# Kernel tuning notes

Measured on AMD Instinct MI355X. Metric: run time of the kernel, lower is better.

Reference implementation:

```python
import jax, jax.numpy as jnp
import numpy as np

M = 8192      # nodes
D = 128       # feature dim
DEG = 32      # neighbors per node


def setup_inputs() -> dict:
    key = jax.random.key(0)
    ks = jax.random.split(key, 6)
    z = jax.random.normal(ks[0], (M, D), dtype=jnp.float32)
    # deterministic, duplicate-free edge list: node i -> (i+1..i+DEG) mod M
    src = jnp.repeat(jnp.arange(M, dtype=jnp.int64), DEG)
    dst = (src + jnp.tile(jnp.arange(1, DEG + 1, dtype=jnp.int64), M)) % M
    edge_index = jnp.stack([src, dst], axis=0)  # [2, M*DEG]
    s = 1.0 / np.sqrt(D)
    Wg = jax.random.normal(ks[1], (D, D), dtype=jnp.float32) * s
    Wc = jax.random.normal(ks[2], (D, D), dtype=jnp.float32) * s
    Wq = jax.random.normal(ks[3], (D, D), dtype=jnp.float32) * s
    Wk = jax.random.normal(ks[4], (D, D), dtype=jnp.float32) * s
    a = jax.random.normal(ks[5], (2 * D,), dtype=jnp.float32)
    return {"z": z, "edge_index": edge_index, "Wg": Wg, "Wc": Wc,
            "Wq": Wq, "Wk": Wk, "a": a}


def reference(z, edge_index, Wg, Wc, Wq, Wk, a):
    m, d = z.shape
    wg = z @ Wg.T                              # [m, d]
    src, dst = edge_index[0], edge_index[1]
    a_src, a_dst = a[:d], a[d:]
    # per-edge score: leaky_relu(a . [wg[i], wg[j]]) = leaky_relu(a1.wg[i] + a2.wg[j])
    scores = jax.nn.leaky_relu((wg @ a_src)[src] + (wg @ a_dst)[dst])  # [E]
    # softmax over each source node's neighbors (segment softmax)
    smax = jax.ops.segment_max(scores, src, num_segments=m)
    ex = jnp.exp(scores - smax[src])
    denom = jax.ops.segment_sum(ex, src, num_segments=m)
    alpha = ex / denom[src]                    # [E]
    # scatter-aggregate: local[i] = sum_j alpha_ij * wg[j]
    local = jax.ops.segment_sum(alpha[:, None] * wg[dst], src, num_segments=m)
    # dense global attention branch
    q = z @ Wq.T
    k = z @ Wk.T
    beta = jax.nn.softmax(q @ k.T / jnp.sqrt(jnp.float32(d)), axis=-1)  # [m, m]
    global_msg = beta @ (z @ Wc.T)
    return jax.nn.leaky_relu(local + global_msg + z)
```

## Files before the change

### kernel.cpp

```cpp
#include <hip/hip_runtime.h>

#define MM 8192
#define DD 128
#define DEG 32
#define KSPLIT 8
#define BK 64
#define NTILE 16
#define NB 16
#define RSTAGE 48

typedef __attribute__((ext_vector_type(8))) _Float16 h8;
typedef __attribute__((ext_vector_type(4))) float f4;
typedef __attribute__((ext_vector_type(4))) unsigned int u4;
typedef __attribute__((ext_vector_type(4))) short s4;

__device__ __forceinline__ unsigned short f2h(float f) {
  _Float16 h = (_Float16)f;
  return __builtin_bit_cast(unsigned short, h);
}

__device__ __forceinline__ void lds_dma16(const unsigned short* gptr, unsigned short* lptr) {
  __builtin_amdgcn_global_load_lds(
      (const __attribute__((address_space(1))) unsigned int*)gptr,
      (__attribute__((address_space(3))) unsigned int*)lptr, 16, 0, 0);
}

__global__ __launch_bounds__(256) void proj_kernel(
    const float* __restrict__ z, const float* __restrict__ Wg,
    const float* __restrict__ Wc, const float* __restrict__ Wq,
    const float* __restrict__ Wk, const float* __restrict__ a,
    float* __restrict__ wg, unsigned short* __restrict__ qb,
    unsigned short* __restrict__ kb, unsigned short* __restrict__ ct,
    float* __restrict__ sg, float* __restrict__ sd)
{
  __shared__ unsigned short zt[64 * 136];
  __shared__ unsigned short wt[128 * 136];
  const int mode = blockIdx.y;
  const float* __restrict__ W = (mode == 0) ? Wg : (mode == 1) ? Wq : (mode == 2) ? Wk : Wc;
  const int r0 = blockIdx.x * 64;
  const int tid = threadIdx.x;

  #pragma unroll
  for (int it = 0; it < 8; ++it) {
    int id = tid + it * 256, row = id >> 5, c4 = (id & 31) * 4;
    f4 v = *(const f4*)(z + (r0 + row) * DD + c4);
    s4 sv = {(short)f2h(v.x), (short)f2h(v.y), (short)f2h(v.z), (short)f2h(v.w)};
    *(s4*)&zt[row * 136 + c4] = sv;
  }
  #pragma unroll
  for (int it = 0; it < 16; ++it) {
    int id = tid + it * 256, row = id >> 5, c4 = (id & 31) * 4;
    f4 v = *(const f4*)(W + row * DD + c4);
    s4 sv = {(short)f2h(v.x), (short)f2h(v.y), (short)f2h(v.z), (short)f2h(v.w)};
    *(s4*)&wt[row * 136 + c4] = sv;
  }
  __syncthreads();

  const int lane = tid & 63, w = tid >> 6, n = lane & 15, quad = lane >> 4;
  h8 afr[4];
  #pragma unroll
  for (int kt = 0; kt < 4; ++kt)
    afr[kt] = *(const h8*)&zt[(16 * w + n) * 136 + kt * 32 + quad * 8];

  f4 acc[8];
  const f4 fzero = {0.f, 0.f, 0.f, 0.f};
  #pragma unroll
  for (int nt = 0; nt < 8; ++nt) {
    f4 c = fzero;
    #pragma unroll
    for (int kt = 0; kt < 4; ++kt) {
      h8 b = *(const h8*)&wt[(16 * nt + n) * 136 + kt * 32 + quad * 8];
      c = __builtin_amdgcn_mfma_f32_16x16x32_f16(afr[kt], b, c, 0, 0, 0);
    }
    acc[nt] = c;
  }

  if (mode == 0) {
    #pragma unroll
    for (int nt = 0; nt < 8; ++nt)
      #pragma unroll
      for (int r = 0; r < 4; ++r)
        wg[(r0 + 16 * w + quad * 4 + r) * DD + 16 * nt + n] = acc[nt][r];
    float av[8], bv[8];
    #pragma unroll
    for (int nt = 0; nt < 8; ++nt) { av[nt] = a[16 * nt + n]; bv[nt] = a[DD + 16 * nt + n]; }
    #pragma unroll
    for (int r = 0; r < 4; ++r) {
      float s1 = 0.f, s2 = 0.f;
      #pragma unroll
      for (int nt = 0; nt < 8; ++nt) { s1 += acc[nt][r] * av[nt]; s2 += acc[nt][r] * bv[nt]; }
      s1 += __shfl_xor(s1, 1); s1 += __shfl_xor(s1, 2); s1 += __shfl_xor(s1, 4); s1 += __shfl_xor(s1, 8);
      s2 += __shfl_xor(s2, 1); s2 += __shfl_xor(s2, 2); s2 += __shfl_xor(s2, 4); s2 += __shfl_xor(s2, 8);
      if (n == 0) {
        int g = r0 + 16 * w + quad * 4 + r;
        sg[g] = s1; sd[g] = s2;
      }
    }
  } else if (mode == 1) {
    const float qscale = 0.12752551286084110f;
    #pragma unroll
    for (int nt = 0; nt < 8; ++nt)
      #pragma unroll
      for (int r = 0; r < 4; ++r)
        qb[(r0 + 16 * w + quad * 4 + r) * DD + 16 * nt + n] = f2h(acc[nt][r] * qscale);
  } else if (mode == 2) {
    #pragma unroll
    for (int nt = 0; nt < 8; ++nt)
      #pragma unroll
      for (int r = 0; r < 4; ++r)
        kb[(r0 + 16 * w + quad * 4 + r) * DD + 16 * nt + n] = f2h(acc[nt][r]);
  } else {
    __syncthreads();
    #pragma unroll
    for (int nt = 0; nt < 8; ++nt)
      #pragma unroll
      for (int r = 0; r < 4; ++r)
        wt[(16 * nt + n) * 80 + 16 * w + quad * 4 + r] = f2h(acc[nt][r]);
    __syncthreads();
    #pragma unroll
    for (int it = 0; it < 4; ++it) {
      int idx = tid + it * 256, d = idx >> 3, c8 = (idx & 7) * 8;
      u4 v = *(const u4*)&wt[d * 80 + c8];
      *(u4*)(ct + (size_t)d * MM + r0 + c8) = v;
    }
  }
}

__global__ __launch_bounds__(256, 2) void flash_kernel(
    const unsigned short* __restrict__ qb, const unsigned short* __restrict__ kb,
    const unsigned short* __restrict__ ct, unsigned short* __restrict__ Opart,
    float* __restrict__ Lpart)
{
  __shared__ unsigned short sh[37376];
  const int bid = blockIdx.x + (blockIdx.y << 6);
  const int ck = bid & 7, qt = bid >> 3;
  const int tid = threadIdx.x, lane = tid & 63, w = tid >> 6;
  const int n = lane & 15, quad = lane >> 4;
  const int qr0 = qt * 128;

  #pragma unroll
  for (int it = 0; it < 8; ++it)
    lds_dma16(qb + (qr0 + it * 16 + n) * DD + w * 32 + quad * 8,
              &sh[(it * 256 + tid) * 8]);
  __syncthreads();
  h8 aq[2][4];
  #pragma unroll
  for (int mt = 0; mt < 2; ++mt)
    #pragma unroll
    for (int kt = 0; kt < 4; ++kt)
      aq[mt][kt] = *(const h8*)&sh[((w * 2 + mt) * 4 + kt) * 512 + lane * 8];
  __syncthreads();

  const unsigned short* kp = kb + (size_t)(ck * 1024 + 4 * n) * DD + w * 32 + quad * 8;
  const unsigned short* vp = ct + (size_t)(16 * (w >> 1) + n) * MM + ck * 1024 + (w & 1) * 32 + quad * 8;

  #pragma unroll
  for (int it = 0; it < 4; ++it)
    lds_dma16(kp + it * DD, &sh[(it * 256 + tid) * 8]);
  #pragma unroll
  for (int it = 0; it < 4; ++it)
    lds_dma16(vp + (size_t)it * 32 * MM, &sh[8192 + (it * 256 + tid) * 8]);

  f4 acc_o[2][8];
  const f4 fzero = {0.f, 0.f, 0.f, 0.f};
  #pragma unroll
  for (int mt = 0; mt < 2; ++mt)
    #pragma unroll
    for (int dt = 0; dt < 8; ++dt) acc_o[mt][dt] = fzero;
  float l_r[2][4] = {{0.f, 0.f, 0.f, 0.f}, {0.f, 0.f, 0.f, 0.f}};
  const int pbase = 32768 + w * 1152;

  for (int t = 0; t < NTILE; ++t) {
    __syncthreads();
    const int cur = (t & 1) * 16384;

    if (t < NTILE - 1) {
      const int nb = ((t + 1) & 1) * 16384;
      const unsigned short* kpn = kp + (size_t)(t + 1) * BK * DD;
      const unsigned short* vpn = vp + (t + 1) * BK;
      #pragma unroll
      for (int it = 0; it < 4; ++it)
        lds_dma16(kpn + it * DD, &sh[nb + (it * 256 + tid) * 8]);
      #pragma unroll
      for (int it = 0; it < 4; ++it)
        lds_dma16(vpn + (size_t)it * 32 * MM, &sh[nb + 8192 + (it * 256 + tid) * 8]);
    }

    f4 accs[2][4];
    #pragma unroll
    for (int mt = 0; mt < 2; ++mt)
      #pragma unroll
      for (int nt = 0; nt < 4; ++nt) accs[mt][nt] = fzero;
    #pragma unroll
    for (int nt = 0; nt < 4; ++nt) {
      #pragma unroll
      for (int kt = 0; kt < 4; ++kt) {
        h8 bk = *(const h8*)&sh[cur + nt * 2048 + kt * 512 + lane * 8];
        accs[0][nt] = __builtin_amdgcn_mfma_f32_16x16x32_f16(aq[0][kt], bk, accs[0][nt], 0, 0, 0);
        accs[1][nt] = __builtin_amdgcn_mfma_f32_16x16x32_f16(aq[1][kt], bk, accs[1][nt], 0, 0, 0);
      }
    }

    h8 ap[2][2];
    #pragma unroll
    for (int mt = 0; mt < 2; ++mt) {
      #pragma unroll
      for (int r = 0; r < 4; ++r) {
        float p0 = exp2f(fminf(accs[mt][0][r], 14.4269504f));
        float p1 = exp2f(fminf(accs[mt][1][r], 14.4269504f));
        float p2 = exp2f(fminf(accs[mt][2][r], 14.4269504f));
        float p3 = exp2f(fminf(accs[mt][3][r], 14.4269504f));
        l_r[mt][r] += (p0 + p1) + (p2 + p3);
        auto pk0 = __builtin_amdgcn_cvt_pkrtz(p0, p1);
        auto pk1 = __builtin_amdgcn_cvt_pkrtz(p2, p3);
        uint2 pv2; pv2.x = __builtin_bit_cast(unsigned int, pk0);
        pv2.y = __builtin_bit_cast(unsigned int, pk1);
        *(uint2*)&sh[pbase + (quad * 4 + r) * 72 + n * 4] = pv2;
      }
      ap[mt][0] = *(const h8*)&sh[pbase + n * 72 + quad * 8];
      ap[mt][1] = *(const h8*)&sh[pbase + n * 72 + 32 + quad * 8];
    }

    #pragma unroll
    for (int dt = 0; dt < 8; ++dt) {
      #pragma unroll
      for (int k2 = 0; k2 < 2; ++k2) {
        h8 bv = *(const h8*)&sh[cur + 8192 + dt * 1024 + k2 * 512 + lane * 8];
        acc_o[0][dt] = __builtin_amdgcn_mfma_f32_16x16x32_f16(ap[0][k2], bv, acc_o[0][dt], 0, 0, 0);
        acc_o[1][dt] = __builtin_amdgcn_mfma_f32_16x16x32_f16(ap[1][k2], bv, acc_o[1][dt], 0, 0, 0);
      }
    }
  }

  #pragma unroll
  for (int mt = 0; mt < 2; ++mt)
    #pragma unroll
    for (int r = 0; r < 4; ++r) {
      float lv = l_r[mt][r];
      lv += __shfl_xor(lv, 1); lv += __shfl_xor(lv, 2);
      lv += __shfl_xor(lv, 4); lv += __shfl_xor(lv, 8);
      int g = qr0 + w * 32 + mt * 16 + quad * 4 + r;
      if (n == 0) __builtin_nontemporal_store(lv, &Lpart[ck * MM + g]);
      #pragma unroll
      for (int dt = 0; dt < 8; ++dt)
        __builtin_nontemporal_store(f2h(acc_o[mt][dt][r]),
                                    &Opart[((size_t)ck * MM + g) * DD + 16 * dt + n]);
    }
}

__global__ __launch_bounds__(256) void merge_kernel(
    const int* __restrict__ ei, const float* __restrict__ wg,
    const float* __restrict__ sg, const float* __restrict__ sd,
    const unsigned short* __restrict__ Opart, const float* __restrict__ Lpart,
    const float* __restrict__ z, float* __restrict__ out)
{
  __shared__ float rows_s[RSTAGE * 132];
  __shared__ float sc_s[NB][DEG];
  __shared__ float alpha_s[NB][DEG];
  __shared__ int idx_s[NB][DEG];
  const int tid = threadIdx.x;
  const int i0 = blockIdx.x * NB;

  #pragma unroll
  for (int it = 0; it < 6; ++it) {
    int idx = tid + it * 256;
    int r = idx >> 5, c4 = (idx & 31) * 4;
    int grow = (i0 + 1 + r) & (MM - 1);
    *(f4*)&rows_s[r * 132 + c4] = *(const f4*)(wg + (size_t)grow * DD + c4);
  }
  #pragma unroll
  for (int it = 0; it < 2; ++it) {
    int e = tid + it * 256;
    int nj = e >> 5, j = e & 31;
    int i = i0 + nj;
    int dstj = ei[MM * DEG + i * DEG + j];
    float s = sg[i] + sd[dstj];
    sc_s[nj][j] = s > 0.f ? s : 0.01f * s;
    idx_s[nj][j] = (dstj - (i0 + 1)) & (MM - 1);
  }
  __syncthreads();

  const int ni = tid >> 4, l16 = tid & 15;
  {
    float s0 = sc_s[ni][l16], s1 = sc_s[ni][l16 + 16];
    float mx = fmaxf(s0, s1);
    mx = fmaxf(mx, __shfl_xor(mx, 1)); mx = fmaxf(mx, __shfl_xor(mx, 2));
    mx = fmaxf(mx, __shfl_xor(mx, 4)); mx = fmaxf(mx, __shfl_xor(mx, 8));
    float p0 = __expf(s0 - mx), p1 = __expf(s1 - mx);
    float sum = p0 + p1;
    sum += __shfl_xor(sum, 1); sum += __shfl_xor(sum, 2);
    sum += __shfl_xor(sum, 4); sum += __shfl_xor(sum, 8);
    float inv = 1.f / sum;
    alpha_s[ni][l16] = p0 * inv;
    alpha_s[ni][l16 + 16] = p1 * inv;
  }

  const int d0 = l16 * 8;
  const int i = i0 + ni;
  float acc[8] = {0.f, 0.f, 0.f, 0.f, 0.f, 0.f, 0.f, 0.f};
  #pragma unroll 4
  for (int j = 0; j < DEG; ++j) {
    float al = alpha_s[ni][j];
    int r = idx_s[ni][j];
    if (r < RSTAGE) {
      const float* src = &rows_s[r * 132 + d0];
      #pragma unroll
      for (int q = 0; q < 8; ++q) acc[q] += al * src[q];
    } else {
      const float* src = wg + (size_t)((i0 + 1 + r) & (MM - 1)) * DD + d0;
      #pragma unroll
      for (int q = 0; q < 8; ++q) acc[q] += al * src[q];
    }
  }

  float l = 0.f;
  float o[8] = {0.f, 0.f, 0.f, 0.f, 0.f, 0.f, 0.f, 0.f};
  #pragma unroll
  for (int ck = 0; ck < KSPLIT; ++ck) {
    l += __builtin_nontemporal_load(&Lpart[ck * MM + i]);
    h8 v = __builtin_nontemporal_load((const h8*)(Opart + ((size_t)ck * MM + i) * DD + d0));
    #pragma unroll
    for (int q = 0; q < 8; ++q) o[q] += (float)v[q];
  }
  float inv = 1.0f / l;
  const float* zp = z + (size_t)i * DD + d0;
  float* op = out + (size_t)i * DD + d0;
  #pragma unroll
  for (int q = 0; q < 8; ++q) {
    float r = o[q] * inv + acc[q] + zp[q];
    op[q] = r > 0.f ? r : 0.01f * r;
  }
}

extern "C" void kernel_launch(void* const* d_in, const int* in_sizes, int n_in,
                              void* d_out, int out_size, void* d_ws, size_t ws_size,
                              hipStream_t stream) {
  const float* z  = (const float*)d_in[0];
  const int*   ei = (const int*)d_in[1];
  const float* Wg = (const float*)d_in[2];
  const float* Wc = (const float*)d_in[3];
  const float* Wq = (const float*)d_in[4];
  const float* Wk = (const float*)d_in[5];
  const float* a  = (const float*)d_in[6];
  float* out = (float*)d_out;
  char* ws = (char*)d_ws;

  float*          wg    = (float*)(ws + 0);
  unsigned short* qb    = (unsigned short*)(ws + (4 << 20));
  unsigned short* kb    = (unsigned short*)(ws + (6 << 20));
  unsigned short* ct    = (unsigned short*)(ws + (8 << 20));
  float*          sg    = (float*)(ws + (10 << 20));
  float*          sd    = (float*)(ws + (10 << 20) + (64 << 10));
  unsigned short* Opart = (unsigned short*)(ws + (11 << 20));
  float*          Lpart = (float*)(ws + (27 << 20));

  proj_kernel<<<dim3(128, 4), 256, 0, stream>>>(z, Wg, Wc, Wq, Wk, a, wg, qb, kb, ct, sg, sd);
  flash_kernel<<<dim3(64, KSPLIT), 256, 0, stream>>>(qb, kb, ct, Opart, Lpart);
  merge_kernel<<<512, 256, 0, stream>>>(ei, wg, sg, sd, Opart, Lpart, z, out);
}
```

Before: 133.4 us.

## Use packed fp16 conversion, regular stores, simpler flash grid, vectorized merge gather

Several small changes land together. The projection kernel now converts fp32 to fp16 with packed cvt_pkrtz (round toward zero) instead of per-element casts. The flash kernel takes its split index directly from blockIdx.y instead of decoding a flattened block id, which changes how blocks are ordered across the grid. Opart/Lpart stores and loads switch from nontemporal to regular accesses so the partials can stay in cache for the merge kernel, and the merge kernel's neighbor aggregation uses a single pointer select with f4 vector loads instead of a branch. The rounding mode of the z/W conversion changes slightly.

New measurement: 131.2 us. No clear change (-1.6%).

```diff
diff --git a/kernel.cpp b/kernel.cpp
--- a/kernel.cpp
+++ b/kernel.cpp
@@ -10,13 +10,17 @@
 #define RSTAGE 48
 
 typedef __attribute__((ext_vector_type(8))) _Float16 h8;
+typedef __attribute__((ext_vector_type(2))) _Float16 h2;
 typedef __attribute__((ext_vector_type(4))) float f4;
 typedef __attribute__((ext_vector_type(4))) unsigned int u4;
-typedef __attribute__((ext_vector_type(4))) short s4;
 
 __device__ __forceinline__ unsigned short f2h(float f) {
   _Float16 h = (_Float16)f;
   return __builtin_bit_cast(unsigned short, h);
+}
+
+__device__ __forceinline__ unsigned int pkrtz(float a, float b) {
+  return __builtin_bit_cast(unsigned int, __builtin_amdgcn_cvt_pkrtz(a, b));
 }
 
 __device__ __forceinline__ void lds_dma16(const unsigned short* gptr, unsigned short* lptr) {
@@ -44,15 +48,15 @@
   for (int it = 0; it < 8; ++it) {
     int id = tid + it * 256, row = id >> 5, c4 = (id & 31) * 4;
     f4 v = *(const f4*)(z + (r0 + row) * DD + c4);
-    s4 sv = {(short)f2h(v.x), (short)f2h(v.y), (short)f2h(v.z), (short)f2h(v.w)};
-    *(s4*)&zt[row * 136 + c4] = sv;
+    uint2 pk; pk.x = pkrtz(v.x, v.y); pk.y = pkrtz(v.z, v.w);
+    *(uint2*)&zt[row * 136 + c4] = pk;
   }
   #pragma unroll
   for (int it = 0; it < 16; ++it) {
     int id = tid + it * 256, row = id >> 5, c4 = (id & 31) * 4;
     f4 v = *(const f4*)(W + row * DD + c4);
-    s4 sv = {(short)f2h(v.x), (short)f2h(v.y), (short)f2h(v.z), (short)f2h(v.w)};
-    *(s4*)&wt[row * 136 + c4] = sv;
+    uint2 pk; pk.x = pkrtz(v.x, v.y); pk.y = pkrtz(v.z, v.w);
+    *(uint2*)&wt[row * 136 + c4] = pk;
   }
   __syncthreads();
 
@@ -132,15 +136,15 @@
     float* __restrict__ Lpart)
 {
   __shared__ unsigned short sh[37376];
-  const int bid = blockIdx.x + (blockIdx.y << 6);
-  const int ck = bid & 7, qt = bid >> 3;
+  const int bx = blockIdx.x, ck = blockIdx.y;
   const int tid = threadIdx.x, lane = tid & 63, w = tid >> 6;
   const int n = lane & 15, quad = lane >> 4;
-  const int qr0 = qt * 128;
+  const int ln = n, lq = quad;
+  const int qr0 = bx * 128;
 
   #pragma unroll
   for (int it = 0; it < 8; ++it)
-    lds_dma16(qb + (qr0 + it * 16 + n) * DD + w * 32 + quad * 8,
+    lds_dma16(qb + (qr0 + it * 16 + ln) * DD + w * 32 + lq * 8,
               &sh[(it * 256 + tid) * 8]);
   __syncthreads();
   h8 aq[2][4];
@@ -151,8 +155,8 @@
       aq[mt][kt] = *(const h8*)&sh[((w * 2 + mt) * 4 + kt) * 512 + lane * 8];
   __syncthreads();
 
-  const unsigned short* kp = kb + (size_t)(ck * 1024 + 4 * n) * DD + w * 32 + quad * 8;
-  const unsigned short* vp = ct + (size_t)(16 * (w >> 1) + n) * MM + ck * 1024 + (w & 1) * 32 + quad * 8;
+  const unsigned short* kp = kb + (size_t)(ck * 1024 + 4 * ln) * DD + w * 32 + lq * 8;
+  const unsigned short* vp = ct + (size_t)(16 * (w >> 1) + ln) * MM + ck * 1024 + (w & 1) * 32 + lq * 8;
 
   #pragma unroll
   for (int it = 0; it < 4; ++it)
@@ -211,11 +215,8 @@
         float p2 = exp2f(fminf(accs[mt][2][r], 14.4269504f));
         float p3 = exp2f(fminf(accs[mt][3][r], 14.4269504f));
         l_r[mt][r] += (p0 + p1) + (p2 + p3);
-        auto pk0 = __builtin_amdgcn_cvt_pkrtz(p0, p1);
-        auto pk1 = __builtin_amdgcn_cvt_pkrtz(p2, p3);
-        uint2 pv2; pv2.x = __builtin_bit_cast(unsigned int, pk0);
-        pv2.y = __builtin_bit_cast(unsigned int, pk1);
-        *(uint2*)&sh[pbase + (quad * 4 + r) * 72 + n * 4] = pv2;
+        uint2 pv; pv.x = pkrtz(p0, p1); pv.y = pkrtz(p2, p3);
+        *(uint2*)&sh[pbase + (quad * 4 + r) * 72 + n * 4] = pv;
       }
       ap[mt][0] = *(const h8*)&sh[pbase + n * 72 + quad * 8];
       ap[mt][1] = *(const h8*)&sh[pbase + n * 72 + 32 + quad * 8];
@@ -240,11 +241,10 @@
       lv += __shfl_xor(lv, 1); lv += __shfl_xor(lv, 2);
       lv += __shfl_xor(lv, 4); lv += __shfl_xor(lv, 8);
       int g = qr0 + w * 32 + mt * 16 + quad * 4 + r;
-      if (n == 0) __builtin_nontemporal_store(lv, &Lpart[ck * MM + g]);
+      if (n == 0) Lpart[ck * MM + g] = lv;
       #pragma unroll
       for (int dt = 0; dt < 8; ++dt)
-        __builtin_nontemporal_store(f2h(acc_o[mt][dt][r]),
-                                    &Opart[((size_t)ck * MM + g) * DD + 16 * dt + n]);
+        Opart[((size_t)ck * MM + g) * DD + 16 * dt + n] = f2h(acc_o[mt][dt][r]);
     }
 }
 
@@ -297,28 +297,25 @@
 
   const int d0 = l16 * 8;
   const int i = i0 + ni;
-  float acc[8] = {0.f, 0.f, 0.f, 0.f, 0.f, 0.f, 0.f, 0.f};
+  f4 a0 = {0.f, 0.f, 0.f, 0.f}, a1 = {0.f, 0.f, 0.f, 0.f};
   #pragma unroll 4
   for (int j = 0; j < DEG; ++j) {
     float al = alpha_s[ni][j];
     int r = idx_s[ni][j];
-    if (r < RSTAGE) {
-      const float* src = &rows_s[r * 132 + d0];
-      #pragma unroll
-      for (int q = 0; q < 8; ++q) acc[q] += al * src[q];
-    } else {
-      const float* src = wg + (size_t)((i0 + 1 + r) & (MM - 1)) * DD + d0;
-      #pragma unroll
-      for (int q = 0; q < 8; ++q) acc[q] += al * src[q];
-    }
+    const f4* src = (r < RSTAGE)
+        ? (const f4*)&rows_s[r * 132 + d0]
+        : (const f4*)(wg + (size_t)((i0 + 1 + r) & (MM - 1)) * DD + d0);
+    f4 v0 = src[0], v1 = src[1];
+    a0 += v0 * al;
+    a1 += v1 * al;
   }
 
   float l = 0.f;
   float o[8] = {0.f, 0.f, 0.f, 0.f, 0.f, 0.f, 0.f, 0.f};
   #pragma unroll
   for (int ck = 0; ck < KSPLIT; ++ck) {
-    l += __builtin_nontemporal_load(&Lpart[ck * MM + i]);
-    h8 v = __builtin_nontemporal_load((const h8*)(Opart + ((size_t)ck * MM + i) * DD + d0));
+    l += Lpart[ck * MM + i];
+    h8 v = *(const h8*)(Opart + ((size_t)ck * MM + i) * DD + d0);
     #pragma unroll
     for (int q = 0; q < 8; ++q) o[q] += (float)v[q];
   }
@@ -327,7 +324,8 @@
   float* op = out + (size_t)i * DD + d0;
   #pragma unroll
   for (int q = 0; q < 8; ++q) {
-    float r = o[q] * inv + acc[q] + zp[q];
+    float ac = (q < 4) ? a0[q] : a1[q - 4];
+    float r = o[q] * inv + ac + zp[q];
     op[q] = r > 0.f ? r : 0.01f * r;
   }
 }
```
